# Kernel tuning notes

Measured on AMD Instinct MI355X. Metric: run time of the kernel, lower is better.

The kernel has to match this reference:

```python
import jax, jax.numpy as jnp
import numpy as np

BATCH, IN_DIM, UNITS = 1048576, 128, 128


def setup_inputs() -> dict:
    key = jax.random.key(0)
    kx, ks, kv = jax.random.split(key, 3)
    x = jax.random.normal(kx, (BATCH, IN_DIM), dtype=jnp.float32)
    # s_factors ~ N(mu=1.0, sigma=0.1) in the original init
    s = 1.0 + 0.1 * jax.random.normal(ks, (IN_DIM,), dtype=jnp.float32)
    V = jax.random.normal(kv, (IN_DIM, UNITS), dtype=jnp.float32) * (1.0 / np.sqrt(IN_DIM))
    bias = jnp.zeros((UNITS,), dtype=jnp.float32)
    return {"x": x, "s": s, "V": V, "bias": bias}


def reference(x, s, V, bias):
    # W = diag(exp(s)) @ V  ==  exp(s)[:, None] * V  (row-wise scale)
    W = jnp.exp(s)[:, None] * V  # [in_dim, units]
    return jnp.tanh(x @ W + bias)  # [batch, units]
```

## Files before the change

kernel.cpp:

```cpp
#include <hip/hip_runtime.h>
#include <math.h>


typedef _Float16 half8 __attribute__((ext_vector_type(8)));
typedef float float4v __attribute__((ext_vector_type(4)));

#define RWF_BATCH   1048576
#define RWF_K       128
#define RWF_N       128
#define RWF_TILE_M  64
#define RWF_NTILES  (RWF_BATCH / RWF_TILE_M)
#define RWF_GRID    2048

__global__ void rwf_setup_w(const float* __restrict__ s,
                            const float* __restrict__ V,
                            _Float16* __restrict__ wsT) {
    int t = blockIdx.x * blockDim.x + threadIdx.x;
    int i = t >> 7;
    int j = t & 127;
    float w = expf(s[i]) * V[t];
    wsT[j * 128 + i] = (_Float16)w;
}

__global__ __launch_bounds__(256, 4) void rwf_main(
    const float* __restrict__ x,
    const float* __restrict__ bias,
    const _Float16* __restrict__ wsT,
    float* __restrict__ out)
{
    const int lane = threadIdx.x & 63;
    const int wave = threadIdx.x >> 6;
    const int ln15 = lane & 15;
    const int quad = lane >> 4;
    const int wcol = wave * 32;

    half8 bh[4][2];
    #pragma unroll
    for (int ks = 0; ks < 4; ++ks) {
        #pragma unroll
        for (int nt = 0; nt < 2; ++nt) {
            int n = wcol + nt * 16 + ln15;
            bh[ks][nt] = *(const half8*)(wsT + n * 128 + ks * 32 + quad * 8);
        }
    }

    float bv[2];
    #pragma unroll
    for (int nt = 0; nt < 2; ++nt) bv[nt] = bias[wcol + nt * 16 + ln15];

    const int laneoff = ln15 * RWF_K + quad * 8;

    for (int tile = blockIdx.x; tile < RWF_NTILES; tile += gridDim.x) {
        const float* xb = x + (size_t)tile * RWF_TILE_M * RWF_K;

        float4v acc[4][2];
        #pragma unroll
        for (int mt = 0; mt < 4; ++mt)
            #pragma unroll
            for (int nt = 0; nt < 2; ++nt) {
                acc[mt][nt][0] = bv[nt];
                acc[mt][nt][1] = bv[nt];
                acc[mt][nt][2] = bv[nt];
                acc[mt][nt][3] = bv[nt];
            }

        #pragma unroll
        for (int ks = 0; ks < 4; ++ks) {
            half8 a[4];
            #pragma unroll
            for (int mt = 0; mt < 4; ++mt) {
                const float* p = xb + mt * 16 * RWF_K + ks * 32 + laneoff;
                float4v u0 = *(const float4v*)p;
                float4v u1 = *(const float4v*)(p + 4);
                half8 av;
                av[0] = (_Float16)u0[0]; av[1] = (_Float16)u0[1];
                av[2] = (_Float16)u0[2]; av[3] = (_Float16)u0[3];
                av[4] = (_Float16)u1[0]; av[5] = (_Float16)u1[1];
                av[6] = (_Float16)u1[2]; av[7] = (_Float16)u1[3];
                a[mt] = av;
            }
            #pragma unroll
            for (int mt = 0; mt < 4; ++mt) {
                #pragma unroll
                for (int nt = 0; nt < 2; ++nt) {
                    acc[mt][nt] = __builtin_amdgcn_mfma_f32_16x16x32_f16(
                        a[mt], bh[ks][nt], acc[mt][nt], 0, 0, 0);
                }
            }
        }

        const int row0 = tile * RWF_TILE_M + quad * 4;
        const int col0 = wcol + ln15;
        #pragma unroll
        for (int mt = 0; mt < 4; ++mt) {
            #pragma unroll
            for (int nt = 0; nt < 2; ++nt) {
                #pragma unroll
                for (int r = 0; r < 4; ++r) {
                    float z = acc[mt][nt][r];
                    float e = __expf(2.0f * z);
                    float o = 1.0f - 2.0f * __builtin_amdgcn_rcpf(e + 1.0f);
                    __builtin_nontemporal_store(
                        o, out + (size_t)(row0 + mt * 16 + r) * RWF_N
                               + col0 + nt * 16);
                }
            }
        }
    }
}

extern "C" void kernel_launch(void* const* d_in, const int* in_sizes, int n_in,
                              void* d_out, int out_size, void* d_ws, size_t ws_size,
                              hipStream_t stream) {
    const float* x    = (const float*)d_in[0];
    const float* s    = (const float*)d_in[1];
    const float* V    = (const float*)d_in[2];
    const float* bias = (const float*)d_in[3];
    float* out        = (float*)d_out;
    _Float16* wsT     = (_Float16*)d_ws;

    rwf_setup_w<<<(RWF_K * RWF_N) / 256, 256, 0, stream>>>(s, V, wsT);
    rwf_main<<<RWF_GRID, 256, 0, stream>>>(x, bias, wsT, out);
}
```

Before: 988.0 us.

## Double-buffer x tiles into LDS via async global_load_lds with contiguous block ranges

Each block now processes a contiguous range of 32-row tiles, prefetching two tiles ahead into a double-buffered LDS area using direct global-to-LDS loads. Waves then read their A fragments from LDS instead of doing strided per-lane global loads. The goal is to overlap the streaming of x with MFMA and tanh work and to get fully coalesced loads. Costs include barriers every tile, a smaller tile per iteration, a hand-written vmcnt wait that must match the outstanding store/load counts, and losing nontemporal stores.

```diff
diff --git a/kernel.cpp b/kernel.cpp
--- a/kernel.cpp
+++ b/kernel.cpp
@@ -8,9 +8,10 @@
 #define RWF_BATCH   1048576
 #define RWF_K       128
 #define RWF_N       128
-#define RWF_TILE_M  64
+#define RWF_TILE_M  32
 #define RWF_NTILES  (RWF_BATCH / RWF_TILE_M)
 #define RWF_GRID    2048
+#define RWF_TPB     (RWF_NTILES / RWF_GRID)
 
 __global__ void rwf_setup_w(const float* __restrict__ s,
                             const float* __restrict__ V,
@@ -28,6 +29,8 @@
     const _Float16* __restrict__ wsT,
     float* __restrict__ out)
 {
+    __shared__ float lds[2][RWF_TILE_M * RWF_K];
+
     const int lane = threadIdx.x & 63;
     const int wave = threadIdx.x >> 6;
     const int ln15 = lane & 15;
@@ -48,14 +51,35 @@
     #pragma unroll
     for (int nt = 0; nt < 2; ++nt) bv[nt] = bias[wcol + nt * 16 + ln15];
 
-    const int laneoff = ln15 * RWF_K + quad * 8;
+#define RWF_STAGE(buf_, tile_) do {                                          \
+    const float* _src = x + (size_t)(tile_) * (RWF_TILE_M * RWF_K);          \
+    _Pragma("unroll")                                                        \
+    for (int _j = 0; _j < 4; ++_j) {                                         \
+        const int _c = wave * 4 + _j;                                        \
+        __builtin_amdgcn_global_load_lds(                                    \
+            (const __attribute__((address_space(1))) void*)                  \
+                (_src + _c * 256 + lane * 4),                                \
+            (__attribute__((address_space(3))) void*)                        \
+                (&lds[(buf_)][_c * 256]),                                    \
+            16, 0, 0);                                                       \
+    }                                                                        \
+} while (0)
 
-    for (int tile = blockIdx.x; tile < RWF_NTILES; tile += gridDim.x) {
-        const float* xb = x + (size_t)tile * RWF_TILE_M * RWF_K;
+    const int t0 = blockIdx.x * RWF_TPB;
 
-        float4v acc[4][2];
+    RWF_STAGE(0, t0);
+    RWF_STAGE(1, t0 + 1);
+
+    for (int i = 0; i < RWF_TPB; ++i) {
+        const int cur = i & 1;
+        const int t   = t0 + i;
+
+        asm volatile("s_waitcnt vmcnt(4)" ::: "memory");
+        __builtin_amdgcn_s_barrier();
+
+        float4v acc[2][2];
         #pragma unroll
-        for (int mt = 0; mt < 4; ++mt)
+        for (int mt = 0; mt < 2; ++mt)
             #pragma unroll
             for (int nt = 0; nt < 2; ++nt) {
                 acc[mt][nt][0] = bv[nt];
@@ -66,10 +90,11 @@
 
         #pragma unroll
         for (int ks = 0; ks < 4; ++ks) {
-            half8 a[4];
+            half8 a[2];
             #pragma unroll
-            for (int mt = 0; mt < 4; ++mt) {
-                const float* p = xb + mt * 16 * RWF_K + ks * 32 + laneoff;
+            for (int mt = 0; mt < 2; ++mt) {
+                const float* p = &lds[cur][(mt * 16 + ln15) * RWF_K
+                                           + ks * 32 + quad * 8];
                 float4v u0 = *(const float4v*)p;
                 float4v u1 = *(const float4v*)(p + 4);
                 half8 av;
@@ -80,19 +105,17 @@
                 a[mt] = av;
             }
             #pragma unroll
-            for (int mt = 0; mt < 4; ++mt) {
+            for (int mt = 0; mt < 2; ++mt)
                 #pragma unroll
-                for (int nt = 0; nt < 2; ++nt) {
+                for (int nt = 0; nt < 2; ++nt)
                     acc[mt][nt] = __builtin_amdgcn_mfma_f32_16x16x32_f16(
                         a[mt], bh[ks][nt], acc[mt][nt], 0, 0, 0);
-                }
-            }
         }
 
-        const int row0 = tile * RWF_TILE_M + quad * 4;
+        const int row0 = t * RWF_TILE_M + quad * 4;
         const int col0 = wcol + ln15;
         #pragma unroll
-        for (int mt = 0; mt < 4; ++mt) {
+        for (int mt = 0; mt < 2; ++mt) {
             #pragma unroll
             for (int nt = 0; nt < 2; ++nt) {
                 #pragma unroll
@@ -100,13 +123,18 @@
                     float z = acc[mt][nt][r];
                     float e = __expf(2.0f * z);
                     float o = 1.0f - 2.0f * __builtin_amdgcn_rcpf(e + 1.0f);
-                    __builtin_nontemporal_store(
-                        o, out + (size_t)(row0 + mt * 16 + r) * RWF_N
-                               + col0 + nt * 16);
+                    out[(size_t)(row0 + mt * 16 + r) * RWF_N
+                        + col0 + nt * 16] = o;
                 }
             }
         }
+
+        asm volatile("" ::: "memory");
+        __builtin_amdgcn_s_barrier();
+
+        if (i + 2 < RWF_TPB) RWF_STAGE(cur, t + 2);
     }
+#undef RWF_STAGE
 }
 
 extern "C" void kernel_launch(void* const* d_in, const int* in_sizes, int n_in,
```

New measurement: 862.4 us. 12.7% less time.
